# Kernel optimization log

Hardware: AMD Instinct MI355X
Metric: run time of the kernel (lower is better)

The kernel has to match this reference:

```python
import jax, jax.numpy as jnp
import numpy as np

B, S, D, H, E, K = 4, 2048, 1024, 4096, 8, 2

def setup_inputs() -> dict:
    key = jax.random.key(0)
    ks = jax.random.split(key, 7)
    scale = 0.02
    return {
        "x": jax.random.normal(ks[0], (B, S, D), dtype=jnp.float32),
        "Wg": jax.random.normal(ks[1], (D, E), dtype=jnp.float32) * scale,
        "bg": jnp.zeros((E,), dtype=jnp.float32),
        "W1": jax.random.normal(ks[2], (E, D, H), dtype=jnp.float32) * scale,
        "b1": jnp.zeros((E, H), dtype=jnp.float32),
        "W2": jax.random.normal(ks[3], (E, H, D), dtype=jnp.float32) * scale,
        "b2": jnp.zeros((E, D), dtype=jnp.float32),
    }

def reference(x, Wg, bg, W1, b1, W2, b2):
    # Gate: top-k over expert logits, softmax over the k selected logits
    logits = jnp.einsum("bsd,de->bse", x, Wg) + bg          # [B,S,E]
    topv, topi = jax.lax.top_k(logits, K)                     # [B,S,K]
    w = jax.nn.softmax(topv, axis=-1)                          # [B,S,K]
    # Combine weights per expert: sum_k w_k * one_hot(idx_k)
    combine = jnp.sum(jax.nn.one_hot(topi, E, dtype=x.dtype) * w[..., None], axis=-2)  # [B,S,E]
    # Dense per-expert FFN weighted by combine weight (zero weight -> no contribution,
    # identical math to the original masked gather/scatter formulation).
    out = jnp.zeros_like(x)
    for e in range(E):
        h = jax.nn.gelu(jnp.einsum("bsd,dh->bsh", x, W1[e]) + b1[e], approximate=False)
        y = jnp.einsum("bsh,hd->bsd", h, W2[e]) + b2[e]
        out = out + combine[..., e:e + 1] * y
    return out
```

## Files before the change

### kernel.cpp

```cpp
#include <hip/hip_runtime.h>
#include <math.h>

#define TOK   8192
#define DDIM  1024
#define HDIM  4096
#define NEXP  8
#define CAP   17408

typedef __attribute__((ext_vector_type(8))) short  bfrag;
typedef __attribute__((ext_vector_type(4))) float  ffrag;
typedef __attribute__((ext_vector_type(8))) unsigned short us8;

__device__ __forceinline__ unsigned short f2bf(float f) {
  unsigned int u = __float_as_uint(f);
  u = (u + 0x7FFFu + ((u >> 16) & 1u)) >> 16;
  return (unsigned short)u;
}
__device__ __forceinline__ float bf2f(unsigned short u) {
  return __uint_as_float((unsigned int)u << 16);
}

__device__ __forceinline__ void gll16(const void* g, void* l) {
  __builtin_amdgcn_global_load_lds(
      (const __attribute__((address_space(1))) unsigned int*)g,
      (__attribute__((address_space(3))) unsigned int*)l,
      16, 0, 0);
}

__device__ __forceinline__ void local_scan(const int* __restrict__ cnt, int* offs) {
  int o = 0;
#pragma unroll
  for (int e = 0; e < NEXP; ++e) {
    offs[e] = o;
    o += ((cnt[e] + 127) >> 7) << 7;
  }
  offs[NEXP] = o;
}

__global__ __launch_bounds__(256)
void prep_kernel(const float* __restrict__ x,  const float* __restrict__ Wg,
                 const float* __restrict__ bg, unsigned short* __restrict__ xb,
                 int* __restrict__ topi, float* __restrict__ topw,
                 int* __restrict__ cnt, int* __restrict__ token_of,
                 const float* __restrict__ W1, unsigned short* __restrict__ w1b,
                 const float* __restrict__ W2, unsigned short* __restrict__ w2b) {
  __shared__ __align__(16) float T[2 * 4352];
  int tid = threadIdx.x;

  if (blockIdx.x < 256) {
    int* hist = (int*)T;
    if (tid < NEXP) hist[tid] = 0;
    int gid = blockIdx.x * 256 + tid;
    if (gid < CAP) token_of[gid] = -1;
    __syncthreads();

    int w = tid >> 6, l = tid & 63;
    const float4* wg4 = (const float4*)Wg;
#pragma unroll 1
    for (int ti = 0; ti < 8; ++ti) {
      int t = (blockIdx.x * 4 + w) * 8 + ti;
      const float4* xr = (const float4*)(x + (size_t)t * DDIM);
      float acc[8];
#pragma unroll
      for (int e = 0; e < 8; ++e) acc[e] = 0.f;
#pragma unroll
      for (int gi = 0; gi < 2; ++gi) {
        int f = gi * 128 + 2 * l;
        float4 a0 = xr[f], a1 = xr[f + 1];
        us8 o;
        o[0] = (short)f2bf(a0.x); o[1] = (short)f2bf(a0.y);
        o[2] = (short)f2bf(a0.z); o[3] = (short)f2bf(a0.w);
        o[4] = (short)f2bf(a1.x); o[5] = (short)f2bf(a1.y);
        o[6] = (short)f2bf(a1.z); o[7] = (short)f2bf(a1.w);
        *(us8*)&xb[(size_t)t * DDIM + f * 4] = o;
        float xs[8] = { a0.x, a0.y, a0.z, a0.w, a1.x, a1.y, a1.z, a1.w };
        int dbase = f * 4;
#pragma unroll
        for (int c = 0; c < 8; ++c) {
          float4 w0 = wg4[(dbase + c) * 2 + 0];
          float4 w1 = wg4[(dbase + c) * 2 + 1];
          acc[0] += xs[c] * w0.x; acc[1] += xs[c] * w0.y;
          acc[2] += xs[c] * w0.z; acc[3] += xs[c] * w0.w;
          acc[4] += xs[c] * w1.x; acc[5] += xs[c] * w1.y;
          acc[6] += xs[c] * w1.z; acc[7] += xs[c] * w1.w;
        }
      }
#pragma unroll
      for (int off = 32; off >= 1; off >>= 1)
#pragma unroll
        for (int e = 0; e < 8; ++e) acc[e] += __shfl_down(acc[e], off);
      if (l == 0) {
        float v[8];
#pragma unroll
        for (int e = 0; e < 8; ++e) v[e] = acc[e] + bg[e];
        int i0 = 0;
#pragma unroll
        for (int e = 1; e < 8; ++e) if (v[e] > v[i0]) i0 = e;
        int i1 = -1;
#pragma unroll
        for (int e = 0; e < 8; ++e) if (e != i0 && (i1 < 0 || v[e] > v[i1])) i1 = e;
        float e1 = expf(v[i1] - v[i0]);
        float s = 1.f + e1;
        topi[t * 2 + 0] = i0; topi[t * 2 + 1] = i1;
        topw[t * 2 + 0] = 1.f / s; topw[t * 2 + 1] = e1 / s;
        atomicAdd(&hist[i0], 1);
        atomicAdd(&hist[i1], 1);
      }
    }
    __syncthreads();
    if (tid < NEXP) atomicAdd(&cnt[tid], hist[tid]);
    return;
  }

  int orig = blockIdx.x - 256;
  int bid = (orig & 7) * 256 + (orig >> 3);
  const float* in; unsigned short* out; int R, C, tile;
  if (bid < 1024) { in = W1; out = w1b; R = DDIM; C = HDIM; tile = bid; }
  else            { in = W2; out = w2b; R = HDIM; C = DDIM; tile = bid - 1024; }
  int e = tile >> 7;
  int t = tile & 127;
  int tpr = C >> 8;
  int ty = t / tpr, tx = t % tpr;
  size_t bo = (size_t)e * R * C;
  in += bo; out += bo;
  int r0 = ty * 128, c0 = tx * 256;

  int r4 = (tid >> 4) * 4;
  int c4 = (tid & 15) * 4;
  int oc = tid >> 2;
  int kg = (tid & 3) * 16;

  auto ld = [&](int s, float4* v) {
    int rb = r0 + (s >> 2) * 64;
    int cb = c0 + (s & 3) * 64;
    v[0] = *(const float4*)&in[(size_t)(rb + r4 + 0) * C + cb + c4];
    v[1] = *(const float4*)&in[(size_t)(rb + r4 + 1) * C + cb + c4];
    v[2] = *(const float4*)&in[(size_t)(rb + r4 + 2) * C + cb + c4];
    v[3] = *(const float4*)&in[(size_t)(rb + r4 + 3) * C + cb + c4];
  };

  float4 v[4], nv[4];
  ld(0, v);
#pragma unroll
  for (int s = 0; s < 8; ++s) {
    if (s + 1 < 8) ld(s + 1, nv);
    float* Tb = T + (s & 1) * 4352;
    int rb = r0 + (s >> 2) * 64;
    int cb = c0 + (s & 3) * 64;
    float4 t0 = { v[0].x, v[1].x, v[2].x, v[3].x };
    float4 t1 = { v[0].y, v[1].y, v[2].y, v[3].y };
    float4 t2 = { v[0].z, v[1].z, v[2].z, v[3].z };
    float4 t3 = { v[0].w, v[1].w, v[2].w, v[3].w };
    *(float4*)&Tb[(c4 + 0) * 68 + r4] = t0;
    *(float4*)&Tb[(c4 + 1) * 68 + r4] = t1;
    *(float4*)&Tb[(c4 + 2) * 68 + r4] = t2;
    *(float4*)&Tb[(c4 + 3) * 68 + r4] = t3;
    __syncthreads();
    float4 f0 = *(const float4*)&Tb[oc * 68 + kg + 0];
    float4 f1 = *(const float4*)&Tb[oc * 68 + kg + 4];
    float4 f2 = *(const float4*)&Tb[oc * 68 + kg + 8];
    float4 f3 = *(const float4*)&Tb[oc * 68 + kg + 12];
    us8 a, b;
    a[0] = (short)f2bf(f0.x); a[1] = (short)f2bf(f0.y);
    a[2] = (short)f2bf(f0.z); a[3] = (short)f2bf(f0.w);
    a[4] = (short)f2bf(f1.x); a[5] = (short)f2bf(f1.y);
    a[6] = (short)f2bf(f1.z); a[7] = (short)f2bf(f1.w);
    b[0] = (short)f2bf(f2.x); b[1] = (short)f2bf(f2.y);
    b[2] = (short)f2bf(f2.z); b[3] = (short)f2bf(f2.w);
    b[4] = (short)f2bf(f3.x); b[5] = (short)f2bf(f3.y);
    b[6] = (short)f2bf(f3.z); b[7] = (short)f2bf(f3.w);
    size_t sub = ((size_t)(cb >> 6) * (R >> 6) + (rb >> 6)) * 4096;
    *(us8*)&out[sub + oc * 64 + kg + 0] = a;
    *(us8*)&out[sub + oc * 64 + kg + 8] = b;
    v[0] = nv[0]; v[1] = nv[1]; v[2] = nv[2]; v[3] = nv[3];
  }
}

__global__ __launch_bounds__(256) void assign_kernel(const int* __restrict__ topi,
                                                     const int* __restrict__ cnt,
                                                     int* __restrict__ cursor,
                                                     int* __restrict__ row_of,
                                                     int* __restrict__ token_of) {
  int offs[NEXP + 1];
  local_scan(cnt, offs);
  int id = blockIdx.x * 256 + threadIdx.x;
  int e = topi[id];
  int slot = atomicAdd(&cursor[e], 1);
  int row = offs[e] + slot;
  row_of[id] = row;
  token_of[row] = id >> 1;
}

template<bool INDIRECT, bool GELU, bool KSPLIT>
__global__ __launch_bounds__(256)
void moe_gemm(const unsigned short* __restrict__ A,
              const unsigned short* __restrict__ B0,
              const float* __restrict__ bias0,
              unsigned short* __restrict__ out,
              int N, int Kfull,
              const int* __restrict__ cnt,
              const int* __restrict__ token_of) {
  int offsets[NEXP + 1];
  local_scan(cnt, offsets);

  int nwg = gridDim.x * gridDim.y;
  int orig = blockIdx.y * gridDim.x + blockIdx.x;
  int V = nwg >> 3;
  int vid = (orig & 7) * V + (orig >> 3);
  int xcd = vid / V;
  int vloc = vid - xcd * V;
  int P = V / gridDim.x;
  int CW = gridDim.x >= 8 ? 8 : gridDim.x;
  int per = P * CW;
  int g = vloc / per;
  int rem = vloc - g * per;
  int m = rem / CW;
  int bx = g * CW + (rem - m * CW);
  int by = xcd * P + m;

  int kp = 0, koff = 0, Klocal = Kfull;
  if (KSPLIT) {
    kp = bx & 1; bx >>= 1;
    Klocal = Kfull >> 1;
    koff = kp * Klocal;
    out += (size_t)kp * CAP * N;
  }

  int row0 = by * 128;
  if (row0 >= offsets[NEXP]) return;
  int e = 0;
  while (row0 >= offsets[e + 1]) ++e;
  const unsigned short* B = B0 + (size_t)e * N * Kfull;
  const float* bias = bias0 + (size_t)e * N;
  int n0 = bx * 128;

  __shared__ __align__(16) char sm[49152];

  int tid = threadIdx.x;
  int w = tid >> 6, l = tid & 63;
  int lrow = l & 15, kq = l >> 4;
  int wm = w >> 1, wn = w & 1;

  int c2 = (l & 7) ^ (l >> 3);
  int rloc = ((l >> 3) << 1) + (c2 >> 2);
  int ksw = (c2 & 3) * 16;
  int s0 = 2 * w, s1 = 2 * w + 1;

  int gr0 = row0 + s0 * 16 + rloc, gr1 = row0 + s1 * 16 + rloc;
  int ar0, ar1;
  if (INDIRECT) {
    int t0 = token_of[gr0]; ar0 = t0 < 0 ? 0 : t0;
    int t1 = token_of[gr1]; ar1 = t1 < 0 ? 0 : t1;
  } else { ar0 = gr0; ar1 = gr1; }
  const char* srcA0 = (const char*)(A + (size_t)ar0 * Kfull + koff) + ksw;
  const char* srcA1 = (const char*)(A + (size_t)ar1 * Kfull + koff) + ksw;
  auto bsrc = [&](int nloc) -> const char* {
    int n = n0 + nloc;
    return (const char*)B + ((size_t)(n >> 6) * (Kfull >> 6) + (koff >> 6)) * 8192
         + (n & 63) * 128 + ksw;
  };
  const char* srcB0 = bsrc(s0 * 16 + rloc);
  const char* srcB1 = bsrc(s1 * 16 + rloc);

  auto stage = [&](int buf, int k0) {
    int kbA = k0 * 2;
    int kbB = (k0 >> 6) * 8192 + (k0 & 63) * 2;
    gll16(srcA0 + kbA, sm + buf * 8192 + s0 * 1024);
    gll16(srcA1 + kbA, sm + buf * 8192 + s1 * 1024);
    gll16(srcB0 + kbB, sm + 24576 + buf * 8192 + s0 * 1024);
    gll16(srcB1 + kbB, sm + 24576 + buf * 8192 + s1 * 1024);
  };

  int offA[4], offB[4];
#pragma unroll
  for (int i = 0; i < 4; ++i) {
    int ra = wm * 64 + i * 16 + lrow;
    offA[i] = (ra >> 1) * 128 + (((((ra & 1) << 2) + kq) ^ ((ra >> 1) & 7)) << 4);
    int rb = wn * 64 + i * 16 + lrow;
    offB[i] = 24576 + (rb >> 1) * 128 + (((((rb & 1) << 2) + kq) ^ ((rb >> 1) & 7)) << 4);
  }

  ffrag acc[4][4];
#pragma unroll
  for (int i = 0; i < 4; ++i)
#pragma unroll
    for (int j = 0; j < 4; ++j) acc[i][j] = (ffrag){0.f, 0.f, 0.f, 0.f};

  auto compute = [&](int buf) {
    int ab = buf * 8192;
    bfrag a[4], b[4];
#pragma unroll
    for (int i = 0; i < 4; ++i) a[i] = *(const bfrag*)(sm + ab + offA[i]);
#pragma unroll
    for (int j = 0; j < 4; ++j) b[j] = *(const bfrag*)(sm + ab + offB[j]);
#pragma unroll
    for (int i = 0; i < 4; ++i)
#pragma unroll
      for (int j = 0; j < 4; ++j)
        acc[i][j] = __builtin_amdgcn_mfma_f32_16x16x32_bf16(a[i], b[j], acc[i][j], 0, 0, 0);
  };

  stage(0, 0); stage(1, 32);
  asm volatile("s_waitcnt vmcnt(4)" ::: "memory");
  __builtin_amdgcn_s_barrier();

  int nk = Klocal / 32;
  int cur = 0;
  for (int kt = 0; kt < nk; ++kt) {
    int nxt2 = cur + 2; if (nxt2 >= 3) nxt2 -= 3;
    if (kt + 2 < nk) stage(nxt2, (kt + 2) * 32);
    compute(cur);
    if (kt + 1 < nk) {
      if (kt + 2 < nk) { asm volatile("s_waitcnt vmcnt(4)" ::: "memory"); }
      else             { asm volatile("s_waitcnt vmcnt(0)" ::: "memory"); }
    }
    __builtin_amdgcn_s_barrier();
    ++cur; if (cur == 3) cur = 0;
  }

  unsigned short* ht = (unsigned short*)sm;
#pragma unroll
  for (int j = 0; j < 4; ++j) {
    int col = wn * 64 + j * 16 + lrow;
    float bj = (!KSPLIT || kp == 0) ? bias[n0 + col] : 0.0f;
#pragma unroll
    for (int i = 0; i < 4; ++i) {
      int rl = wm * 64 + i * 16 + kq * 4;
#pragma unroll
      for (int r = 0; r < 4; ++r) {
        float v = acc[i][j][r] + bj;
        if (GELU) {
          float z = 1.5957691216f * (v + 0.044715f * v * v * v);
          v = v / (1.0f + __expf(-z));
        }
        ht[(rl + r) * 128 + col] = f2bf(v);
      }
    }
  }
  __syncthreads();
#pragma unroll
  for (int it = 0; it < 8; ++it) {
    int c = it * 256 + tid;
    int row = c >> 4;
    int cc = (c & 15) * 8;
    us8 v = *(const us8*)&ht[row * 128 + cc];
    *(us8*)&out[(size_t)(row0 + row) * N + n0 + cc] = v;
  }
}

__global__ __launch_bounds__(256) void combine_kernel(const unsigned short* __restrict__ y,
                                                      const int* __restrict__ row_of,
                                                      const float* __restrict__ topw,
                                                      float* __restrict__ out) {
  int t = blockIdx.x;
  int r0 = row_of[t * 2 + 0], r1 = row_of[t * 2 + 1];
  float w0 = topw[t * 2 + 0], w1 = topw[t * 2 + 1];
  const size_t P1 = (size_t)CAP * DDIM;
  const ushort4* a0 = (const ushort4*)(y + (size_t)r0 * DDIM);
  const ushort4* a1 = (const ushort4*)(y + P1 + (size_t)r0 * DDIM);
  const ushort4* b0 = (const ushort4*)(y + (size_t)r1 * DDIM);
  const ushort4* b1 = (const ushort4*)(y + P1 + (size_t)r1 * DDIM);
  float4* o = (float4*)(out + (size_t)t * DDIM);
  int i = threadIdx.x;
  ushort4 pa0 = a0[i], pa1 = a1[i], pb0 = b0[i], pb1 = b1[i];
  float4 r = {
    w0 * (bf2f(pa0.x) + bf2f(pa1.x)) + w1 * (bf2f(pb0.x) + bf2f(pb1.x)),
    w0 * (bf2f(pa0.y) + bf2f(pa1.y)) + w1 * (bf2f(pb0.y) + bf2f(pb1.y)),
    w0 * (bf2f(pa0.z) + bf2f(pa1.z)) + w1 * (bf2f(pb0.z) + bf2f(pb1.z)),
    w0 * (bf2f(pa0.w) + bf2f(pa1.w)) + w1 * (bf2f(pb0.w) + bf2f(pb1.w))
  };
  o[i] = r;
}

extern "C" void kernel_launch(void* const* d_in, const int* in_sizes, int n_in,
                              void* d_out, int out_size, void* d_ws, size_t ws_size,
                              hipStream_t stream) {
  const float* x  = (const float*)d_in[0];
  const float* Wg = (const float*)d_in[1];
  const float* bg = (const float*)d_in[2];
  const float* W1 = (const float*)d_in[3];
  const float* b1 = (const float*)d_in[4];
  const float* W2 = (const float*)d_in[5];
  const float* b2 = (const float*)d_in[6];
  float* out = (float*)d_out;

  size_t off = 0;
  char* base = (char*)d_ws;
  auto alloc = [&](size_t bytes) -> void* {
    void* p = base + off;
    off += (bytes + 255) & ~(size_t)255;
    return p;
  };
  unsigned short* xb  = (unsigned short*)alloc((size_t)TOK * DDIM * 2);
  unsigned short* w1b = (unsigned short*)alloc((size_t)NEXP * HDIM * DDIM * 2);
  unsigned short* w2b = (unsigned short*)alloc((size_t)NEXP * DDIM * HDIM * 2);
  unsigned short* h   = (unsigned short*)alloc((size_t)CAP * HDIM * 2);
  unsigned short* y   = (unsigned short*)alloc((size_t)2 * CAP * DDIM * 2);
  int*   topi     = (int*)alloc((size_t)TOK * 2 * 4);
  float* topw     = (float*)alloc((size_t)TOK * 2 * 4);
  int*   row_of   = (int*)alloc((size_t)TOK * 2 * 4);
  int*   token_of = (int*)alloc((size_t)CAP * 4);
  int*   cntcur   = (int*)alloc(64);
  if (off > ws_size) return;

  int* cnt = cntcur;
  int* cursor = cntcur + 8;

  hipMemsetAsync(cntcur, 0, 64, stream);

  prep_kernel<<<2304, 256, 0, stream>>>(x, Wg, bg, xb, topi, topw, cnt, token_of,
                                        W1, w1b, W2, w2b);
  assign_kernel<<<(TOK * 2) / 256, 256, 0, stream>>>(topi, cnt, cursor,
                                                     row_of, token_of);

  moe_gemm<true, true, false><<<dim3(HDIM / 128, CAP / 128), 256, 0, stream>>>(
      xb, w1b, b1, h, HDIM, DDIM, cnt, token_of);
  moe_gemm<false, false, true><<<dim3(16, CAP / 128), 256, 0, stream>>>(
      h, w2b, b2, y, DDIM, HDIM, cnt, token_of);

  combine_kernel<<<TOK, 256, 0, stream>>>(y, row_of, topw, out);
}
```

Measured before the change: 531.6 us.

## Overlap W2 bf16 transpose with first expert GEMM in a union kernel

Splits the weight conversion so the prep kernel only converts W1, and moves W2's fp32-to-bf16 blocked transpose into extra blocks at the front of the first GEMM launch. The aim is to overlap W2 conversion bandwidth with the GEMM1 compute, so it no longer sits on the critical path in prep. The GEMM kernels are specialised into separate non-templated versions with a hand-written XCD-aware tile mapping. The bf16 conversion also switches to the HIP library intrinsic, and an extra barrier is added in the transpose loop.

```diff
diff --git a/kernel.cpp b/kernel.cpp
--- a/kernel.cpp
+++ b/kernel.cpp
@@ -1,4 +1,5 @@
 #include <hip/hip_runtime.h>
+#include <hip/hip_bf16.h>
 #include <math.h>
 
 #define TOK   8192
@@ -12,9 +13,8 @@
 typedef __attribute__((ext_vector_type(8))) unsigned short us8;
 
 __device__ __forceinline__ unsigned short f2bf(float f) {
-  unsigned int u = __float_as_uint(f);
-  u = (u + 0x7FFFu + ((u >> 16) & 1u)) >> 16;
-  return (unsigned short)u;
+  __hip_bfloat16 b = __float2bfloat16(f);
+  return *reinterpret_cast<unsigned short*>(&b);
 }
 __device__ __forceinline__ float bf2f(unsigned short u) {
   return __uint_as_float((unsigned int)u << 16);
@@ -37,94 +37,19 @@
   offs[NEXP] = o;
 }
 
-__global__ __launch_bounds__(256)
-void prep_kernel(const float* __restrict__ x,  const float* __restrict__ Wg,
-                 const float* __restrict__ bg, unsigned short* __restrict__ xb,
-                 int* __restrict__ topi, float* __restrict__ topw,
-                 int* __restrict__ cnt, int* __restrict__ token_of,
-                 const float* __restrict__ W1, unsigned short* __restrict__ w1b,
-                 const float* __restrict__ W2, unsigned short* __restrict__ w2b) {
-  __shared__ __align__(16) float T[2 * 4352];
-  int tid = threadIdx.x;
-
-  if (blockIdx.x < 256) {
-    int* hist = (int*)T;
-    if (tid < NEXP) hist[tid] = 0;
-    int gid = blockIdx.x * 256 + tid;
-    if (gid < CAP) token_of[gid] = -1;
-    __syncthreads();
-
-    int w = tid >> 6, l = tid & 63;
-    const float4* wg4 = (const float4*)Wg;
-#pragma unroll 1
-    for (int ti = 0; ti < 8; ++ti) {
-      int t = (blockIdx.x * 4 + w) * 8 + ti;
-      const float4* xr = (const float4*)(x + (size_t)t * DDIM);
-      float acc[8];
-#pragma unroll
-      for (int e = 0; e < 8; ++e) acc[e] = 0.f;
-#pragma unroll
-      for (int gi = 0; gi < 2; ++gi) {
-        int f = gi * 128 + 2 * l;
-        float4 a0 = xr[f], a1 = xr[f + 1];
-        us8 o;
-        o[0] = (short)f2bf(a0.x); o[1] = (short)f2bf(a0.y);
-        o[2] = (short)f2bf(a0.z); o[3] = (short)f2bf(a0.w);
-        o[4] = (short)f2bf(a1.x); o[5] = (short)f2bf(a1.y);
-        o[6] = (short)f2bf(a1.z); o[7] = (short)f2bf(a1.w);
-        *(us8*)&xb[(size_t)t * DDIM + f * 4] = o;
-        float xs[8] = { a0.x, a0.y, a0.z, a0.w, a1.x, a1.y, a1.z, a1.w };
-        int dbase = f * 4;
-#pragma unroll
-        for (int c = 0; c < 8; ++c) {
-          float4 w0 = wg4[(dbase + c) * 2 + 0];
-          float4 w1 = wg4[(dbase + c) * 2 + 1];
-          acc[0] += xs[c] * w0.x; acc[1] += xs[c] * w0.y;
-          acc[2] += xs[c] * w0.z; acc[3] += xs[c] * w0.w;
-          acc[4] += xs[c] * w1.x; acc[5] += xs[c] * w1.y;
-          acc[6] += xs[c] * w1.z; acc[7] += xs[c] * w1.w;
-        }
-      }
-#pragma unroll
-      for (int off = 32; off >= 1; off >>= 1)
-#pragma unroll
-        for (int e = 0; e < 8; ++e) acc[e] += __shfl_down(acc[e], off);
-      if (l == 0) {
-        float v[8];
-#pragma unroll
-        for (int e = 0; e < 8; ++e) v[e] = acc[e] + bg[e];
-        int i0 = 0;
-#pragma unroll
-        for (int e = 1; e < 8; ++e) if (v[e] > v[i0]) i0 = e;
-        int i1 = -1;
-#pragma unroll
-        for (int e = 0; e < 8; ++e) if (e != i0 && (i1 < 0 || v[e] > v[i1])) i1 = e;
-        float e1 = expf(v[i1] - v[i0]);
-        float s = 1.f + e1;
-        topi[t * 2 + 0] = i0; topi[t * 2 + 1] = i1;
-        topw[t * 2 + 0] = 1.f / s; topw[t * 2 + 1] = e1 / s;
-        atomicAdd(&hist[i0], 1);
-        atomicAdd(&hist[i1], 1);
-      }
-    }
-    __syncthreads();
-    if (tid < NEXP) atomicAdd(&cnt[tid], hist[tid]);
-    return;
-  }
-
-  int orig = blockIdx.x - 256;
-  int bid = (orig & 7) * 256 + (orig >> 3);
-  const float* in; unsigned short* out; int R, C, tile;
-  if (bid < 1024) { in = W1; out = w1b; R = DDIM; C = HDIM; tile = bid; }
-  else            { in = W2; out = w2b; R = HDIM; C = DDIM; tile = bid - 1024; }
+__device__ __forceinline__ void transpose_tile(const float* __restrict__ in0,
+                                               unsigned short* __restrict__ out0,
+                                               int R, int C, int tile, float* T) {
   int e = tile >> 7;
   int t = tile & 127;
   int tpr = C >> 8;
   int ty = t / tpr, tx = t % tpr;
   size_t bo = (size_t)e * R * C;
-  in += bo; out += bo;
+  const float* in = in0 + bo;
+  unsigned short* out = out0 + bo;
   int r0 = ty * 128, c0 = tx * 256;
 
+  int tid = threadIdx.x;
   int r4 = (tid >> 4) * 4;
   int c4 = (tid & 15) * 4;
   int oc = tid >> 2;
@@ -172,8 +97,88 @@
     size_t sub = ((size_t)(cb >> 6) * (R >> 6) + (rb >> 6)) * 4096;
     *(us8*)&out[sub + oc * 64 + kg + 0] = a;
     *(us8*)&out[sub + oc * 64 + kg + 8] = b;
+    __syncthreads();
     v[0] = nv[0]; v[1] = nv[1]; v[2] = nv[2]; v[3] = nv[3];
   }
+}
+
+__global__ __launch_bounds__(256)
+void prep1_kernel(const float* __restrict__ x,  const float* __restrict__ Wg,
+                  const float* __restrict__ bg, unsigned short* __restrict__ xb,
+                  int* __restrict__ topi, float* __restrict__ topw,
+                  int* __restrict__ cnt, int* __restrict__ token_of,
+                  const float* __restrict__ W1, unsigned short* __restrict__ w1b) {
+  __shared__ __align__(16) float T[2 * 4352];
+  int tid = threadIdx.x;
+
+  if (blockIdx.x >= 256) {
+    int orig = blockIdx.x - 256;
+    int bid = (orig & 7) * 128 + (orig >> 3);
+    transpose_tile(W1, w1b, DDIM, HDIM, bid, T);
+    return;
+  }
+
+  int* hist = (int*)T;
+  if (tid < NEXP) hist[tid] = 0;
+  int gid = blockIdx.x * 256 + tid;
+  if (gid < CAP) token_of[gid] = -1;
+  __syncthreads();
+
+  int w = tid >> 6, l = tid & 63;
+  const float4* wg4 = (const float4*)Wg;
+#pragma unroll 1
+  for (int ti = 0; ti < 8; ++ti) {
+    int t = (blockIdx.x * 4 + w) * 8 + ti;
+    const float4* xr = (const float4*)(x + (size_t)t * DDIM);
+    float acc[8];
+#pragma unroll
+    for (int e = 0; e < 8; ++e) acc[e] = 0.f;
+#pragma unroll
+    for (int gi = 0; gi < 2; ++gi) {
+      int f = gi * 128 + 2 * l;
+      float4 a0 = xr[f], a1 = xr[f + 1];
+      us8 o;
+      o[0] = (short)f2bf(a0.x); o[1] = (short)f2bf(a0.y);
+      o[2] = (short)f2bf(a0.z); o[3] = (short)f2bf(a0.w);
+      o[4] = (short)f2bf(a1.x); o[5] = (short)f2bf(a1.y);
+      o[6] = (short)f2bf(a1.z); o[7] = (short)f2bf(a1.w);
+      *(us8*)&xb[(size_t)t * DDIM + f * 4] = o;
+      float xs[8] = { a0.x, a0.y, a0.z, a0.w, a1.x, a1.y, a1.z, a1.w };
+      int dbase = f * 4;
+#pragma unroll
+      for (int c = 0; c < 8; ++c) {
+        float4 w0 = wg4[(dbase + c) * 2 + 0];
+        float4 w1 = wg4[(dbase + c) * 2 + 1];
+        acc[0] += xs[c] * w0.x; acc[1] += xs[c] * w0.y;
+        acc[2] += xs[c] * w0.z; acc[3] += xs[c] * w0.w;
+        acc[4] += xs[c] * w1.x; acc[5] += xs[c] * w1.y;
+        acc[6] += xs[c] * w1.z; acc[7] += xs[c] * w1.w;
+      }
+    }
+#pragma unroll
+    for (int off = 32; off >= 1; off >>= 1)
+#pragma unroll
+      for (int e = 0; e < 8; ++e) acc[e] += __shfl_down(acc[e], off);
+    if (l == 0) {
+      float v[8];
+#pragma unroll
+      for (int e = 0; e < 8; ++e) v[e] = acc[e] + bg[e];
+      int i0 = 0;
+#pragma unroll
+      for (int e = 1; e < 8; ++e) if (v[e] > v[i0]) i0 = e;
+      int i1 = -1;
+#pragma unroll
+      for (int e = 0; e < 8; ++e) if (e != i0 && (i1 < 0 || v[e] > v[i1])) i1 = e;
+      float e1 = expf(v[i1] - v[i0]);
+      float s = 1.f + e1;
+      topi[t * 2 + 0] = i0; topi[t * 2 + 1] = i1;
+      topw[t * 2 + 0] = 1.f / s; topw[t * 2 + 1] = e1 / s;
+      atomicAdd(&hist[i0], 1);
+      atomicAdd(&hist[i1], 1);
+    }
+  }
+  __syncthreads();
+  if (tid < NEXP) atomicAdd(&cnt[tid], hist[tid]);
 }
 
 __global__ __launch_bounds__(256) void assign_kernel(const int* __restrict__ topi,
@@ -191,15 +196,157 @@
   token_of[row] = id >> 1;
 }
 
-template<bool INDIRECT, bool GELU, bool KSPLIT>
 __global__ __launch_bounds__(256)
-void moe_gemm(const unsigned short* __restrict__ A,
-              const unsigned short* __restrict__ B0,
-              const float* __restrict__ bias0,
-              unsigned short* __restrict__ out,
-              int N, int Kfull,
-              const int* __restrict__ cnt,
-              const int* __restrict__ token_of) {
+void gemm1_union(const unsigned short* __restrict__ A,
+                 const unsigned short* __restrict__ B0,
+                 const float* __restrict__ bias0,
+                 unsigned short* __restrict__ hout,
+                 const int* __restrict__ cnt,
+                 const int* __restrict__ token_of,
+                 const float* __restrict__ W2, unsigned short* __restrict__ w2b) {
+  __shared__ __align__(16) char sm[49152];
+  constexpr int N = HDIM, Kfull = DDIM;
+
+  if (blockIdx.x < 1024) {
+    int orig = blockIdx.x;
+    int bid = (orig & 7) * 128 + (orig >> 3);
+    transpose_tile(W2, w2b, HDIM, DDIM, bid, (float*)sm);
+    return;
+  }
+
+  int offsets[NEXP + 1];
+  local_scan(cnt, offsets);
+
+  int orig = blockIdx.x - 1024;
+  int xcd = orig & 7;
+  int vloc = orig >> 3;
+  int g = vloc / 136;
+  int rem = vloc - g * 136;
+  int m = rem >> 3;
+  int bx = g * 8 + (rem & 7);
+  int by = xcd * 17 + m;
+
+  int row0 = by * 128;
+  if (row0 >= offsets[NEXP]) return;
+  int e = 0;
+  while (row0 >= offsets[e + 1]) ++e;
+  const unsigned short* B = B0 + (size_t)e * N * Kfull;
+  const float* bias = bias0 + (size_t)e * N;
+  int n0 = bx * 128;
+
+  int tid = threadIdx.x;
+  int w = tid >> 6, l = tid & 63;
+  int lrow = l & 15, kq = l >> 4;
+  int wm = w >> 1, wn = w & 1;
+
+  int c2 = (l & 7) ^ (l >> 3);
+  int rloc = ((l >> 3) << 1) + (c2 >> 2);
+  int ksw = (c2 & 3) * 16;
+  int s0 = 2 * w, s1 = 2 * w + 1;
+
+  int gr0 = row0 + s0 * 16 + rloc, gr1 = row0 + s1 * 16 + rloc;
+  int t0 = token_of[gr0]; int ar0 = t0 < 0 ? 0 : t0;
+  int t1 = token_of[gr1]; int ar1 = t1 < 0 ? 0 : t1;
+  const char* srcA0 = (const char*)(A + (size_t)ar0 * Kfull) + ksw;
+  const char* srcA1 = (const char*)(A + (size_t)ar1 * Kfull) + ksw;
+  auto bsrc = [&](int nloc) -> const char* {
+    int n = n0 + nloc;
+    return (const char*)B + ((size_t)(n >> 6) * (Kfull >> 6)) * 8192 + (n & 63) * 128 + ksw;
+  };
+  const char* srcB0 = bsrc(s0 * 16 + rloc);
+  const char* srcB1 = bsrc(s1 * 16 + rloc);
+
+  auto stage = [&](int buf, int k0) {
+    int kbA = k0 * 2;
+    int kbB = (k0 >> 6) * 8192 + (k0 & 63) * 2;
+    gll16(srcA0 + kbA, sm + buf * 8192 + s0 * 1024);
+    gll16(srcA1 + kbA, sm + buf * 8192 + s1 * 1024);
+    gll16(srcB0 + kbB, sm + 24576 + buf * 8192 + s0 * 1024);
+    gll16(srcB1 + kbB, sm + 24576 + buf * 8192 + s1 * 1024);
+  };
+
+  int offA[4], offB[4];
+#pragma unroll
+  for (int i = 0; i < 4; ++i) {
+    int ra = wm * 64 + i * 16 + lrow;
+    offA[i] = (ra >> 1) * 128 + (((((ra & 1) << 2) + kq) ^ ((ra >> 1) & 7)) << 4);
+    int rb = wn * 64 + i * 16 + lrow;
+    offB[i] = 24576 + (rb >> 1) * 128 + (((((rb & 1) << 2) + kq) ^ ((rb >> 1) & 7)) << 4);
+  }
+
+  ffrag acc[4][4];
+#pragma unroll
+  for (int i = 0; i < 4; ++i)
+#pragma unroll
+    for (int j = 0; j < 4; ++j) acc[i][j] = (ffrag){0.f, 0.f, 0.f, 0.f};
+
+  auto compute = [&](int buf) {
+    int ab = buf * 8192;
+    bfrag a[4], b[4];
+#pragma unroll
+    for (int i = 0; i < 4; ++i) a[i] = *(const bfrag*)(sm + ab + offA[i]);
+#pragma unroll
+    for (int j = 0; j < 4; ++j) b[j] = *(const bfrag*)(sm + ab + offB[j]);
+#pragma unroll
+    for (int i = 0; i < 4; ++i)
+#pragma unroll
+      for (int j = 0; j < 4; ++j)
+        acc[i][j] = __builtin_amdgcn_mfma_f32_16x16x32_bf16(a[i], b[j], acc[i][j], 0, 0, 0);
+  };
+
+  stage(0, 0); stage(1, 32);
+  asm volatile("s_waitcnt vmcnt(4)" ::: "memory");
+  __builtin_amdgcn_s_barrier();
+
+  const int nk = Kfull / 32;
+  int cur = 0;
+  for (int kt = 0; kt < nk; ++kt) {
+    int nxt2 = cur + 2; if (nxt2 >= 3) nxt2 -= 3;
+    if (kt + 2 < nk) stage(nxt2, (kt + 2) * 32);
+    compute(cur);
+    if (kt + 1 < nk) {
+      if (kt + 2 < nk) { asm volatile("s_waitcnt vmcnt(4)" ::: "memory"); }
+      else             { asm volatile("s_waitcnt vmcnt(0)" ::: "memory"); }
+    }
+    __builtin_amdgcn_s_barrier();
+    ++cur; if (cur == 3) cur = 0;
+  }
+
+  unsigned short* ht = (unsigned short*)sm;
+#pragma unroll
+  for (int j = 0; j < 4; ++j) {
+    int col = wn * 64 + j * 16 + lrow;
+    float bj = bias[n0 + col];
+#pragma unroll
+    for (int i = 0; i < 4; ++i) {
+      int rl = wm * 64 + i * 16 + kq * 4;
+#pragma unroll
+      for (int r = 0; r < 4; ++r) {
+        float v = acc[i][j][r] + bj;
+        float z = 1.5957691216f * (v + 0.044715f * v * v * v);
+        v = v / (1.0f + __expf(-z));
+        ht[(rl + r) * 128 + col] = f2bf(v);
+      }
+    }
+  }
+  __syncthreads();
+#pragma unroll
+  for (int it = 0; it < 8; ++it) {
+    int c = it * 256 + tid;
+    int row = c >> 4;
+    int cc = (c & 15) * 8;
+    us8 v = *(const us8*)&ht[row * 128 + cc];
+    *(us8*)&hout[(size_t)(row0 + row) * N + n0 + cc] = v;
+  }
+}
+
+__global__ __launch_bounds__(256)
+void moe_gemm2(const unsigned short* __restrict__ A,
+               const unsigned short* __restrict__ B0,
+               const float* __restrict__ bias0,
+               unsigned short* __restrict__ out,
+               const int* __restrict__ cnt) {
+  constexpr int N = DDIM, Kfull = HDIM;
   int offsets[NEXP + 1];
   local_scan(cnt, offsets);
 
@@ -218,13 +365,10 @@
   int bx = g * CW + (rem - m * CW);
   int by = xcd * P + m;
 
-  int kp = 0, koff = 0, Klocal = Kfull;
-  if (KSPLIT) {
-    kp = bx & 1; bx >>= 1;
-    Klocal = Kfull >> 1;
-    koff = kp * Klocal;
-    out += (size_t)kp * CAP * N;
-  }
+  int kp = bx & 1; bx >>= 1;
+  const int Klocal = Kfull >> 1;
+  int koff = kp * Klocal;
+  out += (size_t)kp * CAP * N;
 
   int row0 = by * 128;
   if (row0 >= offsets[NEXP]) return;
@@ -247,13 +391,8 @@
   int s0 = 2 * w, s1 = 2 * w + 1;
 
   int gr0 = row0 + s0 * 16 + rloc, gr1 = row0 + s1 * 16 + rloc;
-  int ar0, ar1;
-  if (INDIRECT) {
-    int t0 = token_of[gr0]; ar0 = t0 < 0 ? 0 : t0;
-    int t1 = token_of[gr1]; ar1 = t1 < 0 ? 0 : t1;
-  } else { ar0 = gr0; ar1 = gr1; }
-  const char* srcA0 = (const char*)(A + (size_t)ar0 * Kfull + koff) + ksw;
-  const char* srcA1 = (const char*)(A + (size_t)ar1 * Kfull + koff) + ksw;
+  const char* srcA0 = (const char*)(A + (size_t)gr0 * Kfull + koff) + ksw;
+  const char* srcA1 = (const char*)(A + (size_t)gr1 * Kfull + koff) + ksw;
   auto bsrc = [&](int nloc) -> const char* {
     int n = n0 + nloc;
     return (const char*)B + ((size_t)(n >> 6) * (Kfull >> 6) + (koff >> 6)) * 8192
@@ -304,7 +443,7 @@
   asm volatile("s_waitcnt vmcnt(4)" ::: "memory");
   __builtin_amdgcn_s_barrier();
 
-  int nk = Klocal / 32;
+  const int nk = Klocal / 32;
   int cur = 0;
   for (int kt = 0; kt < nk; ++kt) {
     int nxt2 = cur + 2; if (nxt2 >= 3) nxt2 -= 3;
@@ -322,18 +461,13 @@
 #pragma unroll
   for (int j = 0; j < 4; ++j) {
     int col = wn * 64 + j * 16 + lrow;
-    float bj = (!KSPLIT || kp == 0) ? bias[n0 + col] : 0.0f;
+    float bj = (kp == 0) ? bias[n0 + col] : 0.0f;
 #pragma unroll
     for (int i = 0; i < 4; ++i) {
       int rl = wm * 64 + i * 16 + kq * 4;
 #pragma unroll
       for (int r = 0; r < 4; ++r) {
-        float v = acc[i][j][r] + bj;
-        if (GELU) {
-          float z = 1.5957691216f * (v + 0.044715f * v * v * v);
-          v = v / (1.0f + __expf(-z));
-        }
-        ht[(rl + r) * 128 + col] = f2bf(v);
+        ht[(rl + r) * 128 + col] = f2bf(acc[i][j][r] + bj);
       }
     }
   }
@@ -408,15 +542,14 @@
 
   hipMemsetAsync(cntcur, 0, 64, stream);
 
-  prep_kernel<<<2304, 256, 0, stream>>>(x, Wg, bg, xb, topi, topw, cnt, token_of,
-                                        W1, w1b, W2, w2b);
+  prep1_kernel<<<1280, 256, 0, stream>>>(x, Wg, bg, xb, topi, topw, cnt, token_of,
+                                         W1, w1b);
   assign_kernel<<<(TOK * 2) / 256, 256, 0, stream>>>(topi, cnt, cursor,
                                                      row_of, token_of);
 
-  moe_gemm<true, true, false><<<dim3(HDIM / 128, CAP / 128), 256, 0, stream>>>(
-      xb, w1b, b1, h, HDIM, DDIM, cnt, token_of);
-  moe_gemm<false, false, true><<<dim3(16, CAP / 128), 256, 0, stream>>>(
-      h, w2b, b2, y, DDIM, HDIM, cnt, token_of);
+  gemm1_union<<<1024 + 4352, 256, 0, stream>>>(xb, w1b, b1, h, cnt, token_of,
+                                               W2, w2b);
+  moe_gemm2<<<dim3(16, CAP / 128), 256, 0, stream>>>(h, w2b, b2, y, cnt);
 
   combine_kernel<<<TOK, 256, 0, stream>>>(y, row_of, topw, out);
 }
```

Result: slower. 567.0 us (+6.7%).
